# Optimization experiments

Measured on AMD Instinct MI355X. Metric: run time of the kernel, lower is better.

Reference implementation:

```python
import jax, jax.numpy as jnp
import numpy as np

B, S, D = 4, 2048, 1024
H, HD = 16, 64
FF = 4096
EPS = 1e-5
NEG = -1000000.0


def setup_inputs() -> dict:
    key = jax.random.key(0)
    ks = jax.random.split(key, 12)
    sc = lambda n: 1.0 / np.sqrt(n)
    return {
        "x": jax.random.normal(ks[0], (B, S, D), jnp.float32),
        "valid_lens": jax.random.randint(ks[1], (B,), 1, S, jnp.int32),
        "Wq": jax.random.normal(ks[2], (D, H * HD), jnp.float32) * sc(D),
        "Wk": jax.random.normal(ks[3], (D, H * HD), jnp.float32) * sc(D),
        "Wv": jax.random.normal(ks[4], (D, H * HD), jnp.float32) * sc(D),
        "Wo": jax.random.normal(ks[5], (H * HD, D), jnp.float32) * sc(H * HD),
        "W1": jax.random.normal(ks[6], (D, FF), jnp.float32) * sc(D),
        "b1": jnp.zeros((FF,), jnp.float32),
        "W2": jax.random.normal(ks[7], (FF, D), jnp.float32) * sc(FF),
        "b2": jnp.zeros((D,), jnp.float32),
        "g1": jnp.ones((D,), jnp.float32),
        "beta1": jnp.zeros((D,), jnp.float32),
        "g2": jnp.ones((D,), jnp.float32),
        "beta2": jnp.zeros((D,), jnp.float32),
    }


def _layernorm(x, g, b):
    mu = jnp.mean(x, axis=-1, keepdims=True)
    var = jnp.var(x, axis=-1, keepdims=True)
    return (x - mu) * jax.lax.rsqrt(var + EPS) * g + b


def _encoder_block(x, valid_lens, Wq, Wk, Wv, Wo, W1, b1, W2, b2, g1, beta1, g2, beta2):
    # multi-head attention (vectorized over heads; masked softmax as in original)
    q = (x @ Wq).reshape(B, S, H, HD)
    k = (x @ Wk).reshape(B, S, H, HD)
    v = (x @ Wv).reshape(B, S, H, HD)
    scores = jnp.einsum("bqhd,bkhd->bhqk", q, k) / np.sqrt(HD)
    # mask: key positions >= valid_len[b] set to -1e6 (matches python-loop masking)
    col = jnp.arange(S)[None, None, None, :]           # [1,1,1,S]
    mask = col < valid_lens[:, None, None, None]       # [B,1,1,S]
    scores = jnp.where(mask, scores, NEG)
    w = jax.nn.softmax(scores, axis=-1)
    attn = jnp.einsum("bhqk,bkhd->bqhd", w, v).reshape(B, S, H * HD)
    attn_out = attn @ Wo
    res1 = _layernorm(attn_out + x, g1, beta1)
    ff = jax.nn.relu(res1 @ W1 + b1) @ W2 + b2
    return _layernorm(ff + res1, g2, beta2)


def reference(x, valid_lens, Wq, Wk, Wv, Wo, W1, b1, W2, b2, g1, beta1, g2, beta2):
    return _encoder_block(x, valid_lens, Wq, Wk, Wv, Wo, W1, b1, W2, b2, g1, beta1, g2, beta2)
```

## Files before the change

kernel.cpp:

```cpp
#include <hip/hip_runtime.h>
#include <hip/hip_bf16.h>
#include <stdint.h>

#define BB 4
#define SS 2048
#define DD 1024
#define HH 16
#define HD 64
#define FF 4096
#define MM (BB * SS)
#define BH (BB * HH)

typedef __bf16 bf16x8 __attribute__((ext_vector_type(8)));
typedef float f32x4 __attribute__((ext_vector_type(4)));

static __device__ __forceinline__ unsigned short f2bf(float f) {
  union { float f; unsigned u; } v; v.f = f;
  unsigned r = v.u + 0x7fffu + ((v.u >> 16) & 1u);
  return (unsigned short)(r >> 16);
}

static __device__ __forceinline__ unsigned packbf2(float a, float b) {
  __hip_bfloat162 h = __float22bfloat162_rn(float2{a, b});
  union { __hip_bfloat162 h; unsigned u; } cv; cv.h = h; return cv.u;
}

#define GLD_LDS16(SRC, DST)                                          \
  __builtin_amdgcn_global_load_lds(                                  \
      (const __attribute__((address_space(1))) void*)(SRC),          \
      (__attribute__((address_space(3))) void*)(DST), 16, 0, 0)

__global__ __launch_bounds__(256) void cast_bf16_k(const float* __restrict__ in,
                                                   unsigned short* __restrict__ out) {
  size_t i = ((size_t)blockIdx.x * 256 + threadIdx.x) * 4;
  float4 v = *(const float4*)(in + i);
  ushort4 u;
  u.x = f2bf(v.x); u.y = f2bf(v.y); u.z = f2bf(v.z); u.w = f2bf(v.w);
  *(ushort4*)(out + i) = u;
}

__global__ __launch_bounds__(256) void transpose_cast_k(const float* __restrict__ in,
                                                        unsigned short* __restrict__ out,
                                                        int K, int N) {
  __shared__ float tile[32][33];
  int n0 = blockIdx.x * 32, k0 = blockIdx.y * 32;
  int tx = threadIdx.x, ty = threadIdx.y;
#pragma unroll
  for (int i = 0; i < 32; i += 8)
    tile[ty + i][tx] = in[(size_t)(k0 + ty + i) * N + n0 + tx];
  __syncthreads();
#pragma unroll
  for (int i = 0; i < 32; i += 8)
    out[(size_t)(n0 + ty + i) * K + k0 + tx] = f2bf(tile[tx][ty + i]);
}

template <int EPI>
__global__ __launch_bounds__(256, 2) void gemm_bt(const unsigned short* __restrict__ A,
                                                  const unsigned short* __restrict__ BT,
                                                  const float* __restrict__ bias,
                                                  void* __restrict__ Cout,
                                                  int N, int K) {
  __shared__ __align__(16) unsigned short Al[128 * 64];
  __shared__ __align__(16) unsigned short Bl[128 * 64];
  const int t = threadIdx.x;
  const int w = t >> 6, l = t & 63, lr = l & 15, lg = l >> 4;
  const int gx = gridDim.x;
  int lin = blockIdx.y * gx + blockIdx.x;
  const int nb = gx * gridDim.y;
  lin = (lin & 7) * (nb >> 3) + (lin >> 3);
  const int brow = (lin / gx) << 7, bcol = (lin % gx) << 7;
  const int wr = w >> 1, wc = w & 1;
  f32x4 acc[4][4] = {};

  for (int kt = 0; kt < K; kt += 64) {
    __syncthreads();
#pragma unroll
    for (int is = 0; is < 4; ++is) {
      int c = is * 256 + t;
      int row = c >> 3;
      int js = (c & 7) ^ (row & 7);
      GLD_LDS16(A + (size_t)(brow + row) * K + kt + js * 8,
                &Al[(size_t)(is * 256 + w * 64) * 8]);
      GLD_LDS16(BT + (size_t)(bcol + row) * K + kt + js * 8,
                &Bl[(size_t)(is * 256 + w * 64) * 8]);
    }
    __syncthreads();
#pragma unroll
    for (int kk = 0; kk < 2; ++kk) {
      bf16x8 af[4], bfr[4];
#pragma unroll
      for (int m = 0; m < 4; ++m) {
        int row = wr * 64 + m * 16 + lr;
        af[m] = *(const bf16x8*)&Al[row * 64 + (((kk * 4 + lg) ^ (row & 7)) << 3)];
      }
#pragma unroll
      for (int n = 0; n < 4; ++n) {
        int row = wc * 64 + n * 16 + lr;
        bfr[n] = *(const bf16x8*)&Bl[row * 64 + (((kk * 4 + lg) ^ (row & 7)) << 3)];
      }
#pragma unroll
      for (int m = 0; m < 4; ++m)
#pragma unroll
        for (int n = 0; n < 4; ++n)
          acc[m][n] = __builtin_amdgcn_mfma_f32_16x16x32_bf16(af[m], bfr[n], acc[m][n], 0, 0, 0);
    }
  }

#pragma unroll
  for (int m = 0; m < 4; ++m) {
#pragma unroll
    for (int n = 0; n < 4; ++n) {
      int col = bcol + wc * 64 + n * 16 + lr;
      float bv = 0.f;
      if (EPI == 3 || EPI == 4) bv = bias[col];
#pragma unroll
      for (int i = 0; i < 4; ++i) {
        int row = brow + wr * 64 + m * 16 + lg * 4 + i;
        float v = acc[m][n][i];
        if (EPI == 0) {
          ((float*)Cout)[(size_t)row * N + col] = v;
        } else if (EPI == 3) {
          v += bv; v = v > 0.f ? v : 0.f;
          ((unsigned short*)Cout)[(size_t)row * N + col] = f2bf(v);
        } else if (EPI == 4) {
          v += bv;
          ((float*)Cout)[(size_t)row * N + col] = v;
        } else if (EPI == 5) {
          int b = row >> 11, s = row & 2047;
          int which = col >> 10, cin = col & 1023;
          int h = cin >> 6, hd = cin & 63;
          unsigned short* qb = (unsigned short*)Cout;
          if (which == 0) {
            qb[(((size_t)(b * HH + h)) * SS + s) * HD + hd] = f2bf(v * 0.125f);
          } else if (which == 1) {
            (qb + (size_t)MM * DD)[(((size_t)(b * HH + h)) * SS + s) * HD + hd] = f2bf(v);
          } else {
            (qb + 2 * (size_t)MM * DD)[(((size_t)(b * HH + h)) * HD + hd) * SS + s] = f2bf(v);
          }
        }
      }
    }
  }
}

__global__ __launch_bounds__(256, 4) void attn_kernel(const unsigned short* __restrict__ Q,
                                                      const unsigned short* __restrict__ Kg,
                                                      const unsigned short* __restrict__ VT,
                                                      const int* __restrict__ vlens,
                                                      unsigned short* __restrict__ O) {
  __shared__ __align__(16) unsigned short Kt[64 * 64];
  __shared__ __align__(16) unsigned short Vt[64 * 64];
  const int t = threadIdx.x;
  const int w = t >> 6, l = t & 63, lr = l & 15, lg = l >> 4;
  const int gid = blockIdx.x;
  const int bh = gid & 63, qb = gid >> 6;
  const int b = bh >> 4, h = bh & 15;
  const int q0 = qb << 6;
  const int vl = vlens[b];
  const size_t base = (size_t)bh * SS * HD;

  bf16x8 qf[2];
  {
    const int qrow = q0 + w * 16 + lr;
    qf[0] = *(const bf16x8*)(Q + base + (size_t)qrow * HD + lg * 8);
    qf[1] = *(const bf16x8*)(Q + base + (size_t)qrow * HD + 32 + lg * 8);
  }
  f32x4 o[4] = {};
  float m_r = -3.0e38f, l_r = 0.f;

  const int nkv = (vl + 63) >> 6;
  for (int kbi = 0; kbi < nkv; ++kbi) {
    const int kb = kbi << 6;
    __syncthreads();
#pragma unroll
    for (int is = 0; is < 2; ++is) {
      int c = is * 256 + t;
      int row = c >> 3;
      int js = (c & 7) ^ (row & 7);
      GLD_LDS16(Kg + base + (size_t)(kb + row) * HD + js * 8,
                &Kt[(is * 256 + w * 64) * 8]);
      GLD_LDS16(VT + base + (size_t)row * SS + kb + js * 8,
                &Vt[(is * 256 + w * 64) * 8]);
    }
    __syncthreads();

    f32x4 s[4] = {};
#pragma unroll
    for (int kk = 0; kk < 2; ++kk)
#pragma unroll
      for (int n = 0; n < 4; ++n) {
        int row = n * 16 + lr;
        bf16x8 kf = *(const bf16x8*)&Kt[row * 64 + (((kk * 4 + lg) ^ (row & 7)) << 3)];
        s[n] = __builtin_amdgcn_mfma_f32_16x16x32_bf16(kf, qf[kk], s[n], 0, 0, 0);
      }

    float sv[16];
    const int kbase = kb + lg * 4;
#pragma unroll
    for (int n = 0; n < 4; ++n)
#pragma unroll
      for (int i = 0; i < 4; ++i) {
        float v = s[n][i];
        if (kbase + n * 16 + i >= vl) v = -1.0e30f;
        sv[n * 4 + i] = v;
      }
    float tm[16];
#pragma unroll
    for (int j = 0; j < 16; ++j) tm[j] = sv[j];
#pragma unroll
    for (int st = 8; st >= 1; st >>= 1)
#pragma unroll
      for (int j = 0; j < 8; ++j)
        if (j < st) tm[j] = fmaxf(tm[j], tm[j + st]);
    float rm = tm[0];
    rm = fmaxf(rm, __shfl_xor(rm, 16));
    rm = fmaxf(rm, __shfl_xor(rm, 32));

    if (__any(rm > m_r + 8.f)) {
      float mnew = fmaxf(m_r, rm);
      float alpha = __expf(m_r - mnew);
      m_r = mnew;
      l_r *= alpha;
      float af[4];
#pragma unroll
      for (int i = 0; i < 4; ++i) af[i] = __shfl(alpha, lg * 4 + i);
#pragma unroll
      for (int n = 0; n < 4; ++n)
#pragma unroll
        for (int i = 0; i < 4; ++i) o[n][i] *= af[i];
    }

    float p[16];
#pragma unroll
    for (int j = 0; j < 16; ++j) p[j] = __expf(sv[j] - m_r);
    float ts[16];
#pragma unroll
    for (int j = 0; j < 16; ++j) ts[j] = p[j];
#pragma unroll
    for (int st = 8; st >= 1; st >>= 1)
#pragma unroll
      for (int j = 0; j < 8; ++j)
        if (j < st) ts[j] += ts[j + st];
    float rs = ts[0];
    rs += __shfl_xor(rs, 16);
    rs += __shfl_xor(rs, 32);
    l_r += rs;

    unsigned pd[4][2];
#pragma unroll
    for (int n = 0; n < 4; ++n) {
      pd[n][0] = packbf2(p[n * 4 + 0], p[n * 4 + 1]);
      pd[n][1] = packbf2(p[n * 4 + 2], p[n * 4 + 3]);
    }

#pragma unroll
    for (int kk = 0; kk < 2; ++kk) {
      unsigned pa[4];
#pragma unroll
      for (int jj = 0; jj < 4; ++jj) {
        int src = lr + 16 * (2 * (lg & 1) + (jj >> 1));
        unsigned rlo = __shfl(pd[2 * kk + 0][jj & 1], src);
        unsigned rhi = __shfl(pd[2 * kk + 1][jj & 1], src);
        pa[jj] = (lg & 2) ? rhi : rlo;
      }
      union { unsigned u[4]; bf16x8 v; } pb;
      pb.u[0] = pa[0]; pb.u[1] = pa[1]; pb.u[2] = pa[2]; pb.u[3] = pa[3];
#pragma unroll
      for (int nd = 0; nd < 4; ++nd) {
        int row = nd * 16 + lr;
        bf16x8 vf = *(const bf16x8*)&Vt[row * 64 + (((kk * 4 + lg) ^ (row & 7)) << 3)];
        o[nd] = __builtin_amdgcn_mfma_f32_16x16x32_bf16(pb.v, vf, o[nd], 0, 0, 0);
      }
    }
  }

  float linv[4];
#pragma unroll
  for (int i = 0; i < 4; ++i) linv[i] = 1.f / __shfl(l_r, lg * 4 + i);
#pragma unroll
  for (int nd = 0; nd < 4; ++nd)
#pragma unroll
    for (int i = 0; i < 4; ++i) {
      int qrow = q0 + w * 16 + lg * 4 + i;
      O[((size_t)b * SS + qrow) * DD + h * HD + nd * 16 + lr] = f2bf(o[nd][i] * linv[i]);
    }
}

__global__ __launch_bounds__(256) void ln_kernel(const float* __restrict__ a,
                                                 const float* __restrict__ bsrc,
                                                 const float* __restrict__ g,
                                                 const float* __restrict__ be,
                                                 float* __restrict__ outf,
                                                 unsigned short* __restrict__ outb) {
  const int row = blockIdx.x;
  const int t = threadIdx.x;
  const float4 av = ((const float4*)(a + (size_t)row * DD))[t];
  const float4 bv = ((const float4*)(bsrc + (size_t)row * DD))[t];
  float4 s;
  s.x = av.x + bv.x; s.y = av.y + bv.y; s.z = av.z + bv.z; s.w = av.w + bv.w;
  float sum = s.x + s.y + s.z + s.w;
  float sq = s.x * s.x + s.y * s.y + s.z * s.z + s.w * s.w;
#pragma unroll
  for (int mm = 1; mm < 64; mm <<= 1) {
    sum += __shfl_xor(sum, mm);
    sq += __shfl_xor(sq, mm);
  }
  __shared__ float red[8];
  const int w = t >> 6, l = t & 63;
  if (l == 0) { red[w] = sum; red[4 + w] = sq; }
  __syncthreads();
  sum = red[0] + red[1] + red[2] + red[3];
  sq = red[4] + red[5] + red[6] + red[7];
  const float mu = sum * (1.f / (float)DD);
  const float var = sq * (1.f / (float)DD) - mu * mu;
  const float rs = rsqrtf(var + 1e-5f);
  const float4 gv = ((const float4*)g)[t];
  const float4 bev = ((const float4*)be)[t];
  float4 y;
  y.x = (s.x - mu) * rs * gv.x + bev.x;
  y.y = (s.y - mu) * rs * gv.y + bev.y;
  y.z = (s.z - mu) * rs * gv.z + bev.z;
  y.w = (s.w - mu) * rs * gv.w + bev.w;
  if (outf) ((float4*)(outf + (size_t)row * DD))[t] = y;
  if (outb) {
    ushort4 u;
    u.x = f2bf(y.x); u.y = f2bf(y.y); u.z = f2bf(y.z); u.w = f2bf(y.w);
    ((ushort4*)(outb + (size_t)row * DD))[t] = u;
  }
}

extern "C" void kernel_launch(void* const* d_in, const int* in_sizes, int n_in,
                              void* d_out, int out_size, void* d_ws, size_t ws_size,
                              hipStream_t stream) {
  (void)in_sizes; (void)n_in; (void)out_size; (void)ws_size;
  const float* x = (const float*)d_in[0];
  const int* vlen = (const int*)d_in[1];
  const float* Wq = (const float*)d_in[2];
  const float* Wk = (const float*)d_in[3];
  const float* Wv = (const float*)d_in[4];
  const float* Wo = (const float*)d_in[5];
  const float* W1 = (const float*)d_in[6];
  const float* b1 = (const float*)d_in[7];
  const float* W2 = (const float*)d_in[8];
  const float* b2 = (const float*)d_in[9];
  const float* g1 = (const float*)d_in[10];
  const float* be1 = (const float*)d_in[11];
  const float* g2 = (const float*)d_in[12];
  const float* be2 = (const float*)d_in[13];
  float* out = (float*)d_out;

  char* ws = (char*)d_ws;
  size_t off = 0;
  auto alloc = [&](size_t bytes) {
    char* p = ws + off;
    off += (bytes + 255) & ~(size_t)255;
    return p;
  };
  unsigned short* xb = (unsigned short*)alloc((size_t)MM * DD * 2);
  unsigned short* WqT = (unsigned short*)alloc((size_t)DD * DD * 2);
  unsigned short* WkT = (unsigned short*)alloc((size_t)DD * DD * 2);
  unsigned short* WvT = (unsigned short*)alloc((size_t)DD * DD * 2);
  unsigned short* WoT = (unsigned short*)alloc((size_t)DD * DD * 2);
  unsigned short* W1T = (unsigned short*)alloc((size_t)FF * DD * 2);
  unsigned short* W2T = (unsigned short*)alloc((size_t)DD * FF * 2);
  unsigned short* Qb = (unsigned short*)alloc((size_t)MM * DD * 2);
  unsigned short* Kbb = (unsigned short*)alloc((size_t)MM * DD * 2);
  unsigned short* VTb = (unsigned short*)alloc((size_t)MM * DD * 2);
  unsigned short* attnb = (unsigned short*)alloc((size_t)MM * DD * 2);
  float* proj = (float*)alloc((size_t)MM * DD * 4);
  float* res1f = (float*)alloc((size_t)MM * DD * 4);
  unsigned short* res1b = (unsigned short*)alloc((size_t)MM * DD * 2);
  unsigned short* ff1 = Qb;
  float* ff2 = proj;
  (void)Kbb; (void)VTb;

  cast_bf16_k<<<MM * DD / 1024, 256, 0, stream>>>(x, xb);
  transpose_cast_k<<<dim3(32, 32), dim3(32, 8), 0, stream>>>(Wq, WqT, DD, DD);
  transpose_cast_k<<<dim3(32, 32), dim3(32, 8), 0, stream>>>(Wk, WkT, DD, DD);
  transpose_cast_k<<<dim3(32, 32), dim3(32, 8), 0, stream>>>(Wv, WvT, DD, DD);
  transpose_cast_k<<<dim3(32, 32), dim3(32, 8), 0, stream>>>(Wo, WoT, DD, DD);
  transpose_cast_k<<<dim3(128, 32), dim3(32, 8), 0, stream>>>(W1, W1T, DD, FF);
  transpose_cast_k<<<dim3(32, 128), dim3(32, 8), 0, stream>>>(W2, W2T, FF, DD);

  gemm_bt<5><<<dim3(24, 64), 256, 0, stream>>>(xb, WqT, nullptr, Qb, 3072, DD);

  attn_kernel<<<dim3(2048), 256, 0, stream>>>(Qb, Kbb, VTb, vlen, attnb);

  gemm_bt<0><<<dim3(8, 64), 256, 0, stream>>>(attnb, WoT, nullptr, proj, DD, DD);
  ln_kernel<<<MM, 256, 0, stream>>>(proj, x, g1, be1, res1f, res1b);
  gemm_bt<3><<<dim3(32, 64), 256, 0, stream>>>(res1b, W1T, b1, ff1, FF, DD);
  gemm_bt<4><<<dim3(8, 64), 256, 0, stream>>>(ff1, W2T, b2, ff2, DD, FF);
  ln_kernel<<<MM, 256, 0, stream>>>(ff2, res1f, g2, be2, out, nullptr);
}
```

Measured before the change: 454.9 us.

## Load K/V fragments directly from global memory and remap attention block order

The attention kernel drops the shared-memory staging of K and V tiles and the two barriers per KV step. Each wave now loads its own K and V MFMA fragments straight from global memory into registers. The block index is also permuted so that consecutive blocks are spread across batch-heads, likely to improve XCD/L2 locality. The cost is that each of the four waves re-reads the same K/V tile from global/L2, roughly four times the cache traffic. The register-held fragments also raise register pressure.

```diff
diff --git a/kernel.cpp b/kernel.cpp
--- a/kernel.cpp
+++ b/kernel.cpp
@@ -148,12 +148,11 @@
                                                       const unsigned short* __restrict__ VT,
                                                       const int* __restrict__ vlens,
                                                       unsigned short* __restrict__ O) {
-  __shared__ __align__(16) unsigned short Kt[64 * 64];
-  __shared__ __align__(16) unsigned short Vt[64 * 64];
   const int t = threadIdx.x;
   const int w = t >> 6, l = t & 63, lr = l & 15, lg = l >> 4;
-  const int gid = blockIdx.x;
-  const int bh = gid & 63, qb = gid >> 6;
+  int lin = blockIdx.x;
+  lin = (lin & 7) * 256 + (lin >> 3);
+  const int bh = lin >> 5, qb = lin & 31;
   const int b = bh >> 4, h = bh & 15;
   const int q0 = qb << 6;
   const int vl = vlens[b];
@@ -171,28 +170,27 @@
   const int nkv = (vl + 63) >> 6;
   for (int kbi = 0; kbi < nkv; ++kbi) {
     const int kb = kbi << 6;
-    __syncthreads();
-#pragma unroll
-    for (int is = 0; is < 2; ++is) {
-      int c = is * 256 + t;
-      int row = c >> 3;
-      int js = (c & 7) ^ (row & 7);
-      GLD_LDS16(Kg + base + (size_t)(kb + row) * HD + js * 8,
-                &Kt[(is * 256 + w * 64) * 8]);
-      GLD_LDS16(VT + base + (size_t)row * SS + kb + js * 8,
-                &Vt[(is * 256 + w * 64) * 8]);
-    }
-    __syncthreads();
+    const unsigned short* Kp = Kg + base + (size_t)kb * HD;
+
+    bf16x8 kf[2][4];
+#pragma unroll
+    for (int kk = 0; kk < 2; ++kk)
+#pragma unroll
+      for (int n = 0; n < 4; ++n)
+        kf[kk][n] = *(const bf16x8*)(Kp + (n * 16 + lr) * HD + kk * 32 + lg * 8);
+    bf16x8 vf[2][4];
+#pragma unroll
+    for (int kk = 0; kk < 2; ++kk)
+#pragma unroll
+      for (int nd = 0; nd < 4; ++nd)
+        vf[kk][nd] = *(const bf16x8*)(VT + base + (size_t)(nd * 16 + lr) * SS + kb + kk * 32 + lg * 8);
 
     f32x4 s[4] = {};
 #pragma unroll
     for (int kk = 0; kk < 2; ++kk)
 #pragma unroll
-      for (int n = 0; n < 4; ++n) {
-        int row = n * 16 + lr;
-        bf16x8 kf = *(const bf16x8*)&Kt[row * 64 + (((kk * 4 + lg) ^ (row & 7)) << 3)];
-        s[n] = __builtin_amdgcn_mfma_f32_16x16x32_bf16(kf, qf[kk], s[n], 0, 0, 0);
-      }
+      for (int n = 0; n < 4; ++n)
+        s[n] = __builtin_amdgcn_mfma_f32_16x16x32_bf16(kf[kk][n], qf[kk], s[n], 0, 0, 0);
 
     float sv[16];
     const int kbase = kb + lg * 4;
@@ -266,11 +264,8 @@
       union { unsigned u[4]; bf16x8 v; } pb;
       pb.u[0] = pa[0]; pb.u[1] = pa[1]; pb.u[2] = pa[2]; pb.u[3] = pa[3];
 #pragma unroll
-      for (int nd = 0; nd < 4; ++nd) {
-        int row = nd * 16 + lr;
-        bf16x8 vf = *(const bf16x8*)&Vt[row * 64 + (((kk * 4 + lg) ^ (row & 7)) << 3)];
-        o[nd] = __builtin_amdgcn_mfma_f32_16x16x32_bf16(pb.v, vf, o[nd], 0, 0, 0);
-      }
+      for (int nd = 0; nd < 4; ++nd)
+        o[nd] = __builtin_amdgcn_mfma_f32_16x16x32_bf16(pb.v, vf[kk][nd], o[nd], 0, 0, 0);
     }
   }
 
```

Measured after the change: 709.7 us. +56.0%, slower.

## Process two query tiles per warp in attention to reuse K/V tiles

Applied to the files above, without the earlier changes.

Each attention block now handles 128 query rows, with two 16-row chunks per warp, so every K/V tile loaded into LDS feeds twice the MFMA work and the grid halves. The softmax switches to exp2 by folding log2(e) into the Q scale, and the per-element masking is skipped on fully valid key tiles. The block index is also remapped so neighbouring blocks cover different batches. This cuts global-to-LDS K/V traffic and barrier count per unit of work, at the cost of more registers per thread and fewer blocks available to balance ragged valid lengths.

```diff
diff --git a/kernel.cpp b/kernel.cpp
--- a/kernel.cpp
+++ b/kernel.cpp
@@ -131,7 +131,7 @@
           int h = cin >> 6, hd = cin & 63;
           unsigned short* qb = (unsigned short*)Cout;
           if (which == 0) {
-            qb[(((size_t)(b * HH + h)) * SS + s) * HD + hd] = f2bf(v * 0.125f);
+            qb[(((size_t)(b * HH + h)) * SS + s) * HD + hd] = f2bf(v * 0.18033688011112042f);
           } else if (which == 1) {
             (qb + (size_t)MM * DD)[(((size_t)(b * HH + h)) * SS + s) * HD + hd] = f2bf(v);
           } else {
@@ -153,20 +153,24 @@
   const int t = threadIdx.x;
   const int w = t >> 6, l = t & 63, lr = l & 15, lg = l >> 4;
   const int gid = blockIdx.x;
-  const int bh = gid & 63, qb = gid >> 6;
+  const int r = gid & 63, qb = gid >> 6;
+  const int bh = ((r & 3) << 4) | (r >> 2);
   const int b = bh >> 4, h = bh & 15;
-  const int q0 = qb << 6;
+  const int q0 = qb << 7;
   const int vl = vlens[b];
   const size_t base = (size_t)bh * SS * HD;
 
-  bf16x8 qf[2];
-  {
-    const int qrow = q0 + w * 16 + lr;
-    qf[0] = *(const bf16x8*)(Q + base + (size_t)qrow * HD + lg * 8);
-    qf[1] = *(const bf16x8*)(Q + base + (size_t)qrow * HD + 32 + lg * 8);
-  }
-  f32x4 o[4] = {};
-  float m_r = -3.0e38f, l_r = 0.f;
+  bf16x8 qf[2][2];
+#pragma unroll
+  for (int qc = 0; qc < 2; ++qc) {
+    const int qrow = q0 + w * 32 + qc * 16 + lr;
+    qf[qc][0] = *(const bf16x8*)(Q + base + (size_t)qrow * HD + lg * 8);
+    qf[qc][1] = *(const bf16x8*)(Q + base + (size_t)qrow * HD + 32 + lg * 8);
+  }
+  f32x4 o[2][4] = {};
+  float m_r[2], l_r[2];
+  m_r[0] = m_r[1] = -3.0e38f;
+  l_r[0] = l_r[1] = 0.f;
 
   const int nkv = (vl + 63) >> 6;
   for (int kbi = 0; kbi < nkv; ++kbi) {
@@ -184,106 +188,124 @@
     }
     __syncthreads();
 
-    f32x4 s[4] = {};
+    f32x4 s[2][4] = {};
 #pragma unroll
     for (int kk = 0; kk < 2; ++kk)
 #pragma unroll
       for (int n = 0; n < 4; ++n) {
         int row = n * 16 + lr;
         bf16x8 kf = *(const bf16x8*)&Kt[row * 64 + (((kk * 4 + lg) ^ (row & 7)) << 3)];
-        s[n] = __builtin_amdgcn_mfma_f32_16x16x32_bf16(kf, qf[kk], s[n], 0, 0, 0);
-      }
-
-    float sv[16];
+        s[0][n] = __builtin_amdgcn_mfma_f32_16x16x32_bf16(kf, qf[0][kk], s[0][n], 0, 0, 0);
+        s[1][n] = __builtin_amdgcn_mfma_f32_16x16x32_bf16(kf, qf[1][kk], s[1][n], 0, 0, 0);
+      }
+
+    const bool full = (kb + 64 <= vl);
     const int kbase = kb + lg * 4;
-#pragma unroll
-    for (int n = 0; n < 4; ++n)
-#pragma unroll
-      for (int i = 0; i < 4; ++i) {
-        float v = s[n][i];
-        if (kbase + n * 16 + i >= vl) v = -1.0e30f;
-        sv[n * 4 + i] = v;
-      }
-    float tm[16];
-#pragma unroll
-    for (int j = 0; j < 16; ++j) tm[j] = sv[j];
-#pragma unroll
-    for (int st = 8; st >= 1; st >>= 1)
-#pragma unroll
-      for (int j = 0; j < 8; ++j)
-        if (j < st) tm[j] = fmaxf(tm[j], tm[j + st]);
-    float rm = tm[0];
-    rm = fmaxf(rm, __shfl_xor(rm, 16));
-    rm = fmaxf(rm, __shfl_xor(rm, 32));
-
-    if (__any(rm > m_r + 8.f)) {
-      float mnew = fmaxf(m_r, rm);
-      float alpha = __expf(m_r - mnew);
-      m_r = mnew;
-      l_r *= alpha;
-      float af[4];
-#pragma unroll
-      for (int i = 0; i < 4; ++i) af[i] = __shfl(alpha, lg * 4 + i);
-#pragma unroll
-      for (int n = 0; n < 4; ++n)
-#pragma unroll
-        for (int i = 0; i < 4; ++i) o[n][i] *= af[i];
-    }
-
-    float p[16];
-#pragma unroll
-    for (int j = 0; j < 16; ++j) p[j] = __expf(sv[j] - m_r);
-    float ts[16];
-#pragma unroll
-    for (int j = 0; j < 16; ++j) ts[j] = p[j];
-#pragma unroll
-    for (int st = 8; st >= 1; st >>= 1)
-#pragma unroll
-      for (int j = 0; j < 8; ++j)
-        if (j < st) ts[j] += ts[j + st];
-    float rs = ts[0];
-    rs += __shfl_xor(rs, 16);
-    rs += __shfl_xor(rs, 32);
-    l_r += rs;
-
-    unsigned pd[4][2];
-#pragma unroll
-    for (int n = 0; n < 4; ++n) {
-      pd[n][0] = packbf2(p[n * 4 + 0], p[n * 4 + 1]);
-      pd[n][1] = packbf2(p[n * 4 + 2], p[n * 4 + 3]);
+    unsigned pd[2][4][2];
+
+#pragma unroll
+    for (int qc = 0; qc < 2; ++qc) {
+      float sv[16];
+      if (full) {
+#pragma unroll
+        for (int n = 0; n < 4; ++n)
+#pragma unroll
+          for (int i = 0; i < 4; ++i) sv[n * 4 + i] = s[qc][n][i];
+      } else {
+#pragma unroll
+        for (int n = 0; n < 4; ++n)
+#pragma unroll
+          for (int i = 0; i < 4; ++i) {
+            float v = s[qc][n][i];
+            if (kbase + n * 16 + i >= vl) v = -1.0e30f;
+            sv[n * 4 + i] = v;
+          }
+      }
+      float tm[8];
+#pragma unroll
+      for (int j = 0; j < 8; ++j) tm[j] = fmaxf(sv[j], sv[j + 8]);
+#pragma unroll
+      for (int st = 4; st >= 1; st >>= 1)
+#pragma unroll
+        for (int j = 0; j < 4; ++j)
+          if (j < st) tm[j] = fmaxf(tm[j], tm[j + st]);
+      float rm = tm[0];
+      rm = fmaxf(rm, __shfl_xor(rm, 16));
+      rm = fmaxf(rm, __shfl_xor(rm, 32));
+
+      if (__any(rm > m_r[qc] + 11.5f)) {
+        float mnew = fmaxf(m_r[qc], rm);
+        float alpha = exp2f(m_r[qc] - mnew);
+        m_r[qc] = mnew;
+        l_r[qc] *= alpha;
+        float af[4];
+#pragma unroll
+        for (int i = 0; i < 4; ++i) af[i] = __shfl(alpha, lg * 4 + i);
+#pragma unroll
+        for (int n = 0; n < 4; ++n)
+#pragma unroll
+          for (int i = 0; i < 4; ++i) o[qc][n][i] *= af[i];
+      }
+
+      float p[16];
+#pragma unroll
+      for (int j = 0; j < 16; ++j) p[j] = exp2f(sv[j] - m_r[qc]);
+      float ts[8];
+#pragma unroll
+      for (int j = 0; j < 8; ++j) ts[j] = p[j] + p[j + 8];
+#pragma unroll
+      for (int st = 4; st >= 1; st >>= 1)
+#pragma unroll
+        for (int j = 0; j < 4; ++j)
+          if (j < st) ts[j] += ts[j + st];
+      float rs = ts[0];
+      rs += __shfl_xor(rs, 16);
+      rs += __shfl_xor(rs, 32);
+      l_r[qc] += rs;
+
+#pragma unroll
+      for (int n = 0; n < 4; ++n) {
+        pd[qc][n][0] = packbf2(p[n * 4 + 0], p[n * 4 + 1]);
+        pd[qc][n][1] = packbf2(p[n * 4 + 2], p[n * 4 + 3]);
+      }
     }
 
 #pragma unroll
     for (int kk = 0; kk < 2; ++kk) {
-      unsigned pa[4];
+      union { unsigned u[4]; bf16x8 v; } pb[2];
 #pragma unroll
       for (int jj = 0; jj < 4; ++jj) {
         int src = lr + 16 * (2 * (lg & 1) + (jj >> 1));
-        unsigned rlo = __shfl(pd[2 * kk + 0][jj & 1], src);
-        unsigned rhi = __shfl(pd[2 * kk + 1][jj & 1], src);
-        pa[jj] = (lg & 2) ? rhi : rlo;
-      }
-      union { unsigned u[4]; bf16x8 v; } pb;
-      pb.u[0] = pa[0]; pb.u[1] = pa[1]; pb.u[2] = pa[2]; pb.u[3] = pa[3];
+#pragma unroll
+        for (int qc = 0; qc < 2; ++qc) {
+          unsigned rlo = __shfl(pd[qc][2 * kk + 0][jj & 1], src);
+          unsigned rhi = __shfl(pd[qc][2 * kk + 1][jj & 1], src);
+          pb[qc].u[jj] = (lg & 2) ? rhi : rlo;
+        }
+      }
 #pragma unroll
       for (int nd = 0; nd < 4; ++nd) {
         int row = nd * 16 + lr;
         bf16x8 vf = *(const bf16x8*)&Vt[row * 64 + (((kk * 4 + lg) ^ (row & 7)) << 3)];
-        o[nd] = __builtin_amdgcn_mfma_f32_16x16x32_bf16(pb.v, vf, o[nd], 0, 0, 0);
-      }
-    }
-  }
-
-  float linv[4];
-#pragma unroll
-  for (int i = 0; i < 4; ++i) linv[i] = 1.f / __shfl(l_r, lg * 4 + i);
-#pragma unroll
-  for (int nd = 0; nd < 4; ++nd)
-#pragma unroll
-    for (int i = 0; i < 4; ++i) {
-      int qrow = q0 + w * 16 + lg * 4 + i;
-      O[((size_t)b * SS + qrow) * DD + h * HD + nd * 16 + lr] = f2bf(o[nd][i] * linv[i]);
-    }
+        o[0][nd] = __builtin_amdgcn_mfma_f32_16x16x32_bf16(pb[0].v, vf, o[0][nd], 0, 0, 0);
+        o[1][nd] = __builtin_amdgcn_mfma_f32_16x16x32_bf16(pb[1].v, vf, o[1][nd], 0, 0, 0);
+      }
+    }
+  }
+
+#pragma unroll
+  for (int qc = 0; qc < 2; ++qc) {
+    float linv[4];
+#pragma unroll
+    for (int i = 0; i < 4; ++i) linv[i] = 1.f / __shfl(l_r[qc], lg * 4 + i);
+#pragma unroll
+    for (int nd = 0; nd < 4; ++nd)
+#pragma unroll
+      for (int i = 0; i < 4; ++i) {
+        int qrow = q0 + w * 32 + qc * 16 + lg * 4 + i;
+        O[((size_t)b * SS + qrow) * DD + h * HD + nd * 16 + lr] = f2bf(o[qc][nd][i] * linv[i]);
+      }
+  }
 }
 
 __global__ __launch_bounds__(256) void ln_kernel(const float* __restrict__ a,
@@ -384,7 +406,7 @@
 
   gemm_bt<5><<<dim3(24, 64), 256, 0, stream>>>(xb, WqT, nullptr, Qb, 3072, DD);
 
-  attn_kernel<<<dim3(2048), 256, 0, stream>>>(Qb, Kbb, VTb, vlen, attnb);
+  attn_kernel<<<dim3(1024), 256, 0, stream>>>(Qb, Kbb, VTb, vlen, attnb);
 
   gemm_bt<0><<<dim3(8, 64), 256, 0, stream>>>(attnb, WoT, nullptr, proj, DD, DD);
   ln_kernel<<<MM, 256, 0, stream>>>(proj, x, g1, be1, res1f, res1b);
```

Result: slower. 471.5 us (+3.7%).
